# Performance work log

Hardware: AMD Instinct MI355X
Metric: run time of the kernel (lower is better)

## Reference

```python
import jax, jax.numpy as jnp
import numpy as np

EPS = 1e-5  # BatchNorm eps (torch default)

def _bn(x, gamma, beta):
    # training-mode BatchNorm over the edge/node (leading) axis, biased var
    mean = x.mean(axis=0, keepdims=True)
    var = x.var(axis=0, keepdims=True)
    return (x - mean) * jax.lax.rsqrt(var + EPS) * gamma + beta

def _silu(x):
    return x * jax.nn.sigmoid(x)

def setup_inputs() -> dict:
    N, E, H, NH = 50000, 800000, 128, 4
    HD = H // NH
    key = jax.random.key(0)
    ks = jax.random.split(key, 8)
    x = jax.random.normal(ks[0], (N, H), dtype=jnp.float32)
    weight = jax.random.uniform(ks[1], (N, 1), dtype=jnp.float32)  # positive fraction weights
    src = jax.random.randint(ks[2], (E,), 0, N)
    dst = jax.random.randint(ks[3], (E,), 0, N)
    # f: Linear(2H, 1) + BN(1)
    Wf = jax.random.normal(ks[4], (2 * H, 1), dtype=jnp.float32) * 0.05
    bf = jnp.zeros((1,), jnp.float32)
    f_gamma = jnp.ones((1,), jnp.float32)
    f_beta = jnp.zeros((1,), jnp.float32)
    # g: NH heads of Linear(2H, HD) + BN(HD), stacked on leading head axis
    Wg = jax.random.normal(ks[5], (NH, 2 * H, HD), dtype=jnp.float32) * 0.05
    bg = jnp.zeros((NH, HD), jnp.float32)
    g_gamma = jnp.ones((NH, HD), jnp.float32)
    g_beta = jnp.zeros((NH, HD), jnp.float32)
    # bn_nodes: BN(H)
    n_gamma = jnp.ones((H,), jnp.float32)
    n_beta = jnp.zeros((H,), jnp.float32)
    return dict(x=x, weight=weight, src=src, dst=dst, Wf=Wf, bf=bf,
                f_gamma=f_gamma, f_beta=f_beta, Wg=Wg, bg=bg,
                g_gamma=g_gamma, g_beta=g_beta, n_gamma=n_gamma, n_beta=n_beta)

def reference(x, weight, src, dst, Wf, bf, f_gamma, f_beta, Wg, bg, g_gamma, g_beta, n_gamma, n_beta):
    N = x.shape[0]
    E = src.shape[0]
    # per-edge concat of src/dst node features: [E, 2H]
    hihj = jnp.concatenate([x[src], x[dst]], axis=-1)
    # attention logit f(hihj) = SiLU(BN(Linear)) then exp: [E, 1]
    exp_e = jnp.exp(_silu(_bn(hihj @ Wf + bf, f_gamma, f_beta)))
    # weighted softmax-like normalization over incoming edges of each dst node
    we = weight[src] * exp_e                                   # [E, 1]
    sum_w_exp = jax.ops.segment_sum(we, dst, num_segments=N)   # [N, 1]
    a = we / sum_w_exp[dst]                                    # [E, 1]
    # multi-head message: a_ij * SiLU(BN(Linear_h(hihj))) per head, concat
    z = jnp.einsum('ed,hdk->ehk', hihj, Wg) + bg               # [E, NH, HD]
    z = _silu(_bn(z, g_gamma, g_beta))
    msg = (a[:, :, None] * z).reshape(E, -1)                   # [E, H]
    h = jax.ops.segment_sum(msg, dst, num_segments=N)          # [N, H]
    out = _bn(h, n_gamma, n_beta) + x                          # residual
    return out
```

## Files before the change

### kernel.cpp

```cpp
#include <hip/hip_runtime.h>
#include <hip/hip_bf16.h>
#include <math.h>

#define HDIM 128
#define PAD 64
#define CSTR 16
typedef unsigned short ushort_t;
typedef unsigned int uint_t;
typedef __attribute__((ext_vector_type(8))) short bf16x8;
typedef __attribute__((ext_vector_type(4))) float f32x4;
typedef __attribute__((ext_vector_type(2))) float v2f;

__device__ __forceinline__ float wave_allreduce(float v){
  #pragma unroll
  for (int o = 1; o < 64; o <<= 1) v += __shfl_xor(v, o);
  return v;
}

__device__ __forceinline__ ushort_t f2bf(float f){
  uint_t u = __float_as_uint(f);
  uint_t r = (u + 0x7fffu + ((u >> 16) & 1u)) >> 16;
  return (ushort_t)r;
}

__device__ __forceinline__ v2f bf2(uint_t u){
  v2f r;
  r.x = __uint_as_float(u << 16);
  r.y = __uint_as_float(u & 0xffff0000u);
  return r;
}

__global__ __launch_bounds__(128) void k_wpack(const float* __restrict__ Wg,
    const float* __restrict__ Wf, ushort_t* __restrict__ W3,
    int* __restrict__ cnt, int C){
  int b = blockIdx.x;
  int k = threadIdx.x;
  if (b < 272){
    float val;
    if (b < 128)       val = Wg[(size_t)(b >> 5) * 8192 + k * 32 + (b & 31)];
    else if (b < 256){ int c2 = b - 128;
                       val = Wg[(size_t)(c2 >> 5) * 8192 + (k + 128) * 32 + (c2 & 31)]; }
    else if (b == 256) val = Wf[k];
    else if (b == 257) val = Wf[128 + k];
    else               val = 0.f;
    int idx = (((b >> 4) * 4 + (k >> 5)) * 16 + (b & 15)) * 32 + (k & 31);
    W3[idx] = f2bf(val);
  } else {
    int i = (b - 272) * 128 + k;
    if (i < C) cnt[i] = 0;
  }
}

__global__ __launch_bounds__(256) void k_gemmfill(const float* __restrict__ x,
    const ushort_t* __restrict__ W3, const float* __restrict__ weight,
    ushort_t* __restrict__ Pb, ushort_t* __restrict__ Qb,
    float* __restrict__ v, float2* __restrict__ uw2,
    const int* __restrict__ src, const int* __restrict__ dst,
    int* __restrict__ cnt, int* __restrict__ es,
    int N, int E, int GB){
  __shared__ ushort_t xl[32 * 128];
  __shared__ ushort_t cl[32 * 264];
  if ((int)blockIdx.x < GB){
    int tid = threadIdx.x;
    int n_base = blockIdx.x * 32;
    #pragma unroll
    for (int i = 0; i < 4; ++i){
      int cidx = i * 256 + tid;
      int row = cidx >> 5, ch = cidx & 31;
      int rowc = n_base + row; rowc = rowc < N ? rowc : N - 1;
      float4 a = *(const float4*)(x + (size_t)rowc * HDIM + ch * 4);
      uint_t lo = (uint_t)f2bf(a.x) | ((uint_t)f2bf(a.y) << 16);
      uint_t hi = (uint_t)f2bf(a.z) | ((uint_t)f2bf(a.w) << 16);
      int bo = (row * 256 + ch * 8) ^ ((row & 7) << 4);
      *(uint2*)((char*)xl + bo) = make_uint2(lo, hi);
    }
    __syncthreads();
    int wid = __builtin_amdgcn_readfirstlane(tid >> 6);
    int lane = tid & 63;
    int quad = lane >> 4, col = lane & 15;
    int strip = wid >> 1;
    int half = wid & 1;
    int tbeg = half * 8;
    int ntile = half ? 9 : 8;
    f32x4 acc[9];
    #pragma unroll
    for (int t = 0; t < 9; ++t) acc[t] = (f32x4){0.f, 0.f, 0.f, 0.f};
    int arow = strip * 16 + col;
    #pragma unroll
    for (int kk = 0; kk < 4; ++kk){
      int abyte = (arow * 256 + kk * 64 + quad * 16) ^ ((col & 7) << 4);
      bf16x8 af = *(const bf16x8*)((char*)xl + abyte);
      const ushort_t* wb = W3 + (size_t)(tbeg * 4 + kk) * 512 + col * 32 + quad * 8;
      #pragma unroll
      for (int t = 0; t < 9; ++t){
        if (t < ntile){
          bf16x8 bfr = *(const bf16x8*)(wb + (size_t)t * 2048);
          acc[t] = __builtin_amdgcn_mfma_f32_16x16x32_bf16(af, bfr, acc[t], 0, 0, 0);
        }
      }
    }
    #pragma unroll
    for (int t = 0; t < 8; ++t){
      int ct = tbeg + t;
      #pragma unroll
      for (int r = 0; r < 4; ++r){
        int lr = strip * 16 + quad * 4 + r;
        cl[lr * 264 + ct * 16 + col] = f2bf(acc[t][r]);
      }
    }
    if (half){
      #pragma unroll
      for (int r = 0; r < 4; ++r){
        int n = n_base + strip * 16 + quad * 4 + r;
        if (n < N){
          float val = acc[8][r];
          if (col == 0)      uw2[n] = make_float2(val, weight[n]);
          else if (col == 1) v[n] = val;
        }
      }
    }
    __syncthreads();
    int row = tid >> 3, seg = tid & 7;
    int n = n_base + row;
    if (n < N){
      const ushort_t* s = cl + row * 264 + seg * 32;
      uint4 w0 = *(const uint4*)(s);
      uint4 w1 = *(const uint4*)(s + 8);
      uint4 w2 = *(const uint4*)(s + 16);
      uint4 w3v = *(const uint4*)(s + 24);
      if (seg < 4){
        ushort_t* dp = Pb + (size_t)n * HDIM + seg * 32;
        *(uint4*)(dp) = w0; *(uint4*)(dp + 8) = w1;
        *(uint4*)(dp + 16) = w2; *(uint4*)(dp + 24) = w3v;
      } else {
        ushort_t* dp = Qb + (size_t)n * HDIM + (seg - 4) * 32;
        *(uint4*)(dp) = w0; *(uint4*)(dp + 8) = w1;
        *(uint4*)(dp + 16) = w2; *(uint4*)(dp + 24) = w3v;
      }
    }
  } else {
    int bi = blockIdx.x - GB;
    int part = (int)blockIdx.x & 7;
    int nch = (gridDim.x - GB) >> 3;
    int chunk = bi >> 3;
    int Npp = (N + 7) >> 3;
    int lo = part * Npp;
    int hi = lo + Npp; if (hi > N) hi = N;
    int stride = nch * 256;
    int e = chunk * 256 + threadIdx.x;
#define FILL1(d, s) if ((d) >= lo && (d) < hi){ \
    int c = atomicAdd(&cnt[(size_t)(d) * CSTR], 1); \
    if (c < PAD) es[(size_t)(d) * PAD + c] = (s); }
    for (; e + 7 * stride < E; e += 8 * stride){
      int d0 = dst[e],            d1 = dst[e + stride];
      int d2 = dst[e + 2*stride], d3 = dst[e + 3*stride];
      int d4 = dst[e + 4*stride], d5 = dst[e + 5*stride];
      int d6 = dst[e + 6*stride], d7 = dst[e + 7*stride];
      int s0 = src[e],            s1 = src[e + stride];
      int s2 = src[e + 2*stride], s3 = src[e + 3*stride];
      int s4 = src[e + 4*stride], s5 = src[e + 5*stride];
      int s6 = src[e + 6*stride], s7 = src[e + 7*stride];
      FILL1(d0, s0) FILL1(d1, s1) FILL1(d2, s2) FILL1(d3, s3)
      FILL1(d4, s4) FILL1(d5, s5) FILL1(d6, s6) FILL1(d7, s7)
    }
    for (; e < E; e += stride){
      int d = dst[e];
      FILL1(d, src[e])
    }
#undef FILL1
  }
}

#define SH8(sjv,jj,S) \
  int S##0=__shfl(sjv,(jj)),   S##1=__shfl(sjv,(jj)+1), S##2=__shfl(sjv,(jj)+2), S##3=__shfl(sjv,(jj)+3), \
      S##4=__shfl(sjv,(jj)+4), S##5=__shfl(sjv,(jj)+5), S##6=__shfl(sjv,(jj)+6), S##7=__shfl(sjv,(jj)+7);
#define LD8(S,P) \
  uint_t P##0=Pu[(size_t)S##0*64+lane], P##1=Pu[(size_t)S##1*64+lane], \
         P##2=Pu[(size_t)S##2*64+lane], P##3=Pu[(size_t)S##3*64+lane], \
         P##4=Pu[(size_t)S##4*64+lane], P##5=Pu[(size_t)S##5*64+lane], \
         P##6=Pu[(size_t)S##6*64+lane], P##7=Pu[(size_t)S##7*64+lane];
#define SH4(sjv,jj,S) \
  int S##0=__shfl(sjv,(jj)),   S##1=__shfl(sjv,(jj)+1), S##2=__shfl(sjv,(jj)+2), S##3=__shfl(sjv,(jj)+3);
#define LD4(S,P) \
  uint_t P##0=Pu[(size_t)S##0*64+lane], P##1=Pu[(size_t)S##1*64+lane], \
         P##2=Pu[(size_t)S##2*64+lane], P##3=Pu[(size_t)S##3*64+lane];

__global__ __launch_bounds__(256) void k_gstats(const ushort_t* __restrict__ Pb,
    const ushort_t* __restrict__ Qb, const float* __restrict__ v,
    const float2* __restrict__ uw2, const int* __restrict__ es,
    const int* __restrict__ cnt, float* __restrict__ pstatG, int N){
  int lane = threadIdx.x & 63;
  int wid = __builtin_amdgcn_readfirstlane(threadIdx.x >> 6);
  int part = (int)blockIdx.x & 7;
  int Npp = (N + 7) >> 3;
  int lo = part * Npp;
  int hi = lo + Npp; if (hi > N) hi = N;
  int stp = (gridDim.x >> 3) << 2;
  const uint_t* Pu = (const uint_t*)Pb;
  const uint_t* Qu = (const uint_t*)Qb;
  v2f gs = {0.f,0.f}, gq = {0.f,0.f};
  float fs = 0.f, fq = 0.f;
  int n0 = lo + ((blockIdx.x >> 3) << 2) + wid;
  int n1 = n0 + stp;
  int dnA=0,sjA=0; uint_t qAu=0; float vA=0.f;
  int dnB=0,sjB=0; uint_t qBu=0; float vB=0.f;
  if (n0 < hi){ dnA=cnt[(size_t)n0*CSTR]; sjA=es[(size_t)n0*PAD+lane];
                qAu=Qu[(size_t)n0*64+lane]; vA=v[n0]; }
  if (n1 < hi){ dnB=cnt[(size_t)n1*CSTR]; sjB=es[(size_t)n1*PAD+lane];
                qBu=Qu[(size_t)n1*64+lane]; vB=v[n1]; }
#define GST(p,Sv,Qv) { v2f y=bf2(p); Sv+=y; Qv.x=fmaf(y.x,y.x,Qv.x); Qv.y=fmaf(y.y,y.y,Qv.y); }
#define GED8(P,Sv,Qv) GST(P##0,Sv,Qv) GST(P##1,Sv,Qv) GST(P##2,Sv,Qv) GST(P##3,Sv,Qv) \
                      GST(P##4,Sv,Qv) GST(P##5,Sv,Qv) GST(P##6,Sv,Qv) GST(P##7,Sv,Qv)
#define GED4(P,Sv,Qv) GST(P##0,Sv,Qv) GST(P##1,Sv,Qv) GST(P##2,Sv,Qv) GST(P##3,Sv,Qv)
  while (n0 < hi){
    int m0 = n0 + 2*stp, m1 = n1 + 2*stp;
    int dnC=0,sjC=0; uint_t qCu=0; float vC=0.f;
    int dnD=0,sjD=0; uint_t qDu=0; float vD=0.f;
    if (m0 < hi){ dnC=cnt[(size_t)m0*CSTR]; sjC=es[(size_t)m0*PAD+lane];
                  qCu=Qu[(size_t)m0*64+lane]; vC=v[m0]; }
    if (m1 < hi){ dnD=cnt[(size_t)m1*CSTR]; sjD=es[(size_t)m1*PAD+lane];
                  qDu=Qu[(size_t)m1*64+lane]; vD=v[m1]; }
    int dA = dnA < PAD ? dnA : PAD;
    int dB = (n1 < hi) ? (dnB < PAD ? dnB : PAD) : 0;
    if (lane < dA){ float2 uw = uw2[sjA]; float t = uw.x + vA; fs += t; fq = fmaf(t,t,fq); }
    if (lane < dB){ float2 uw = uw2[sjB]; float t = uw.x + vB; fs += t; fq = fmaf(t,t,fq); }
    v2f qa = bf2(qAu), qb = bf2(qBu);
    v2f SnA={0.f,0.f}, SSA={0.f,0.f}, SnB={0.f,0.f}, SSB={0.f,0.f};
    int j0 = 0, j1 = 0;
    for (; j0 + 7 < dA && j1 + 7 < dB; j0 += 8, j1 += 8){
      SH8(sjA,j0,xa) SH8(sjB,j1,xb)
      LD8(xa,pa) LD8(xb,pb)
      GED8(pa,SnA,SSA) GED8(pb,SnB,SSB)
    }
    for (; j0 + 7 < dA; j0 += 8){ SH8(sjA,j0,xa) LD8(xa,pa) GED8(pa,SnA,SSA) }
    for (; j0 + 3 < dA; j0 += 4){ SH4(sjA,j0,xa) LD4(xa,pa) GED4(pa,SnA,SSA) }
    for (; j0 < dA; ++j0){ int s0=__shfl(sjA,j0); uint_t p0=Pu[(size_t)s0*64+lane]; GST(p0,SnA,SSA) }
    for (; j1 + 7 < dB; j1 += 8){ SH8(sjB,j1,xb) LD8(xb,pb) GED8(pb,SnB,SSB) }
    for (; j1 + 3 < dB; j1 += 4){ SH4(sjB,j1,xb) LD4(xb,pb) GED4(pb,SnB,SSB) }
    for (; j1 < dB; ++j1){ int s0=__shfl(sjB,j1); uint_t p0=Pu[(size_t)s0*64+lane]; GST(p0,SnB,SSB) }
    float dAf = (float)dA, dBf = (float)dB;
    gs.x += SnA.x + SnB.x + dAf*qa.x + dBf*qb.x;
    gs.y += SnA.y + SnB.y + dAf*qa.y + dBf*qb.y;
    gq.x += SSA.x + SSB.x + qa.x*fmaf(dAf,qa.x,2.f*SnA.x) + qb.x*fmaf(dBf,qb.x,2.f*SnB.x);
    gq.y += SSA.y + SSB.y + qa.y*fmaf(dAf,qa.y,2.f*SnA.y) + qb.y*fmaf(dBf,qb.y,2.f*SnB.y);
    n0 = m0; n1 = m1;
    dnA=dnC; sjA=sjC; qAu=qCu; vA=vC;
    dnB=dnD; sjB=sjD; qBu=qDu; vB=vD;
  }
#undef GST
#undef GED8
#undef GED4
  fs = wave_allreduce(fs); fq = wave_allreduce(fq);
  __shared__ float red[4][258];
  red[wid][2*lane]       = gs.x; red[wid][2*lane+1]   = gs.y;
  red[wid][128+2*lane]   = gq.x; red[wid][129+2*lane] = gq.y;
  if (lane == 0){ red[wid][256] = fs; red[wid][257] = fq; }
  __syncthreads();
  for (int c = threadIdx.x; c < 258; c += 256)
    pstatG[(size_t)blockIdx.x * 258 + c] = red[0][c] + red[1][c] + red[2][c] + red[3][c];
}

__global__ __launch_bounds__(256) void k_redfin1(const float* __restrict__ pstatG,
    int NB, const float* __restrict__ g_gamma, const float* __restrict__ g_beta,
    const float* __restrict__ f_gamma, const float* __restrict__ f_beta,
    float* __restrict__ fin, long long E){
  int j = blockIdx.x;
  int c1 = (j < 128) ? j : 256;
  int c2 = (j < 128) ? 128 + j : 257;
  double s1 = 0, s2 = 0;
  for (int b = threadIdx.x; b < NB; b += 256){
    const float* pb = pstatG + (size_t)b * 258;
    s1 += (double)pb[c1]; s2 += (double)pb[c2];
  }
  __shared__ double m1[256], m2[256];
  m1[threadIdx.x] = s1; m2[threadIdx.x] = s2;
  __syncthreads();
  for (int o = 128; o; o >>= 1){
    if (threadIdx.x < o){ m1[threadIdx.x] += m1[threadIdx.x + o];
                          m2[threadIdx.x] += m2[threadIdx.x + o]; }
    __syncthreads();
  }
  if (threadIdx.x == 0){
    double m = m1[0] / (double)E;
    double var = m2[0] / (double)E - m * m;
    if (j < 128){
      float sc = (float)((double)g_gamma[j] / sqrt(var + 1e-5));
      fin[2 + j] = sc; fin[130 + j] = g_beta[j] - (float)m * sc;
    } else {
      float sc = (float)((double)f_gamma[0] / sqrt(var + 1e-5));
      fin[0] = sc; fin[1] = f_beta[0] - (float)m * sc;
    }
  }
}

__global__ __launch_bounds__(256) void k_msg(const ushort_t* __restrict__ Pb,
    const ushort_t* __restrict__ Qb, const float* __restrict__ v,
    const float2* __restrict__ uw2, const int* __restrict__ es,
    const int* __restrict__ cnt, const float* __restrict__ fin,
    float* __restrict__ h, float* __restrict__ pstatH, int N){
  int lane = threadIdx.x & 63;
  int wid = __builtin_amdgcn_readfirstlane(threadIdx.x >> 6);
  int part = (int)blockIdx.x & 7;
  int Npp = (N + 7) >> 3;
  int lo = part * Npp;
  int hi = lo + Npp; if (hi > N) hi = N;
  int stp = (gridDim.x >> 3) << 2;
  const uint_t* Pu = (const uint_t*)Pb;
  const uint_t* Qu = (const uint_t*)Qb;
  float fsc = fin[0], fsh = fin[1];
  v2f gsc = {fin[2 + 2*lane], fin[3 + 2*lane]};
  v2f gsh = {fin[130 + 2*lane], fin[131 + 2*lane]};
  v2f hs = {0.f,0.f}, hq = {0.f,0.f};
  int n0 = lo + ((blockIdx.x >> 3) << 2) + wid;
  int n1 = n0 + stp;
  int dnA=0,sjA=0; uint_t qAu=0; float vA=0.f;
  int dnB=0,sjB=0; uint_t qBu=0; float vB=0.f;
  if (n0 < hi){ dnA=cnt[(size_t)n0*CSTR]; sjA=es[(size_t)n0*PAD+lane];
                qAu=Qu[(size_t)n0*64+lane]; vA=v[n0]; }
  if (n1 < hi){ dnB=cnt[(size_t)n1*CSTR]; sjB=es[(size_t)n1*PAD+lane];
                qBu=Qu[(size_t)n1*64+lane]; vB=v[n1]; }
#define EDGE(p,a,qv,av) { v2f y = (bf2(p) + qv) * gsc + gsh; \
      float e0 = __expf(-y.x), e1 = __expf(-y.y); \
      float d0 = 1.f + e0, d1 = 1.f + e1; \
      float r = __builtin_amdgcn_rcpf(d0 * d1) * (a); \
      av.x = fmaf(y.x * d1, r, av.x); av.y = fmaf(y.y * d0, r, av.y); }
#define ASH8(wjv,jj,A) \
  float A##0=__shfl(wjv,(jj)),   A##1=__shfl(wjv,(jj)+1), A##2=__shfl(wjv,(jj)+2), A##3=__shfl(wjv,(jj)+3), \
        A##4=__shfl(wjv,(jj)+4), A##5=__shfl(wjv,(jj)+5), A##6=__shfl(wjv,(jj)+6), A##7=__shfl(wjv,(jj)+7);
#define ASH4(wjv,jj,A) \
  float A##0=__shfl(wjv,(jj)),   A##1=__shfl(wjv,(jj)+1), A##2=__shfl(wjv,(jj)+2), A##3=__shfl(wjv,(jj)+3);
#define MED8(P,A,qv,av) EDGE(P##0,A##0,qv,av) EDGE(P##1,A##1,qv,av) EDGE(P##2,A##2,qv,av) EDGE(P##3,A##3,qv,av) \
                        EDGE(P##4,A##4,qv,av) EDGE(P##5,A##5,qv,av) EDGE(P##6,A##6,qv,av) EDGE(P##7,A##7,qv,av)
#define MED4(P,A,qv,av) EDGE(P##0,A##0,qv,av) EDGE(P##1,A##1,qv,av) EDGE(P##2,A##2,qv,av) EDGE(P##3,A##3,qv,av)
  while (n0 < hi){
    int m0 = n0 + 2*stp, m1 = n1 + 2*stp;
    int dnC=0,sjC=0; uint_t qCu=0; float vC=0.f;
    int dnD=0,sjD=0; uint_t qDu=0; float vD=0.f;
    if (m0 < hi){ dnC=cnt[(size_t)m0*CSTR]; sjC=es[(size_t)m0*PAD+lane];
                  qCu=Qu[(size_t)m0*64+lane]; vC=v[m0]; }
    if (m1 < hi){ dnD=cnt[(size_t)m1*CSTR]; sjD=es[(size_t)m1*PAD+lane];
                  qDu=Qu[(size_t)m1*64+lane]; vD=v[m1]; }
    int dA = dnA < PAD ? dnA : PAD;
    int dB = (n1 < hi) ? (dnB < PAD ? dnB : PAD) : 0;
    float wjA = 0.f, wjB = 0.f;
    if (lane < dA){ float2 uw = uw2[sjA];
      float tt = fmaf(uw.x + vA, fsc, fsh);
      float sl = tt * __builtin_amdgcn_rcpf(1.f + __expf(-tt));
      wjA = uw.y * __expf(sl); }
    if (lane < dB){ float2 uw = uw2[sjB];
      float tt = fmaf(uw.x + vB, fsc, fsh);
      float sl = tt * __builtin_amdgcn_rcpf(1.f + __expf(-tt));
      wjB = uw.y * __expf(sl); }
    v2f qa = bf2(qAu), qb = bf2(qBu);
    v2f accA = {0.f,0.f}, accB = {0.f,0.f};
    int j0 = 0, j1 = 0;
    for (; j0 + 7 < dA && j1 + 7 < dB; j0 += 8, j1 += 8){
      SH8(sjA,j0,xa) SH8(sjB,j1,xb)
      ASH8(wjA,j0,aa) ASH8(wjB,j1,ab)
      LD8(xa,pa) LD8(xb,pb)
      MED8(pa,aa,qa,accA) MED8(pb,ab,qb,accB)
    }
    for (; j0 + 7 < dA; j0 += 8){ SH8(sjA,j0,xa) ASH8(wjA,j0,aa) LD8(xa,pa) MED8(pa,aa,qa,accA) }
    for (; j0 + 3 < dA; j0 += 4){ SH4(sjA,j0,xa) ASH4(wjA,j0,aa) LD4(xa,pa) MED4(pa,aa,qa,accA) }
    for (; j0 < dA; ++j0){ int s0=__shfl(sjA,j0); float a0=__shfl(wjA,j0);
                           uint_t p0=Pu[(size_t)s0*64+lane]; EDGE(p0,a0,qa,accA) }
    for (; j1 + 7 < dB; j1 += 8){ SH8(sjB,j1,xb) ASH8(wjB,j1,ab) LD8(xb,pb) MED8(pb,ab,qb,accB) }
    for (; j1 + 3 < dB; j1 += 4){ SH4(sjB,j1,xb) ASH4(wjB,j1,ab) LD4(xb,pb) MED4(pb,ab,qb,accB) }
    for (; j1 < dB; ++j1){ int s0=__shfl(sjB,j1); float a0=__shfl(wjB,j1);
                           uint_t p0=Pu[(size_t)s0*64+lane]; EDGE(p0,a0,qb,accB) }
    float swA = wjA, swB = wjB;
    #pragma unroll
    for (int o = 1; o < 64; o <<= 1){ swA += __shfl_xor(swA, o); swB += __shfl_xor(swB, o); }
    float rsA = (dA > 0) ? (1.f / swA) : 0.f;
    float rsB = (dB > 0) ? (1.f / swB) : 0.f;
    accA.x *= rsA; accA.y *= rsA;
    accB.x *= rsB; accB.y *= rsB;
    *(float2*)&h[(size_t)n0 * 128 + 2*lane] = make_float2(accA.x, accA.y);
    hs += accA; hq += accA * accA;
    if (n1 < hi){
      *(float2*)&h[(size_t)n1 * 128 + 2*lane] = make_float2(accB.x, accB.y);
      hs += accB; hq += accB * accB;
    }
    n0 = m0; n1 = m1;
    dnA=dnC; sjA=sjC; qAu=qCu; vA=vC;
    dnB=dnD; sjB=sjD; qBu=qDu; vB=vD;
  }
#undef EDGE
#undef ASH8
#undef ASH4
#undef MED8
#undef MED4
  __shared__ float red[4][256];
  red[wid][2*lane]       = hs.x; red[wid][2*lane+1]   = hs.y;
  red[wid][128+2*lane]   = hq.x; red[wid][129+2*lane] = hq.y;
  __syncthreads();
  int c = threadIdx.x;
  pstatH[(size_t)blockIdx.x * 256 + c] = red[0][c] + red[1][c] + red[2][c] + red[3][c];
}

__global__ __launch_bounds__(256) void k_redfin2(const float* __restrict__ pstatH,
    int NB, const float* __restrict__ n_gamma, const float* __restrict__ n_beta,
    float* __restrict__ fin, int N){
  int j = blockIdx.x;
  double s1 = 0, s2 = 0;
  for (int b = threadIdx.x; b < NB; b += 256){
    const float* pb = pstatH + (size_t)b * 256;
    s1 += (double)pb[j]; s2 += (double)pb[128 + j];
  }
  __shared__ double m1[256], m2[256];
  m1[threadIdx.x] = s1; m2[threadIdx.x] = s2;
  __syncthreads();
  for (int o = 128; o; o >>= 1){
    if (threadIdx.x < o){ m1[threadIdx.x] += m1[threadIdx.x + o];
                          m2[threadIdx.x] += m2[threadIdx.x + o]; }
    __syncthreads();
  }
  if (threadIdx.x == 0){
    double m = m1[0] / (double)N;
    double var = m2[0] / (double)N - m * m;
    float sc = (float)((double)n_gamma[j] / sqrt(var + 1e-5));
    fin[258 + j] = sc; fin[386 + j] = n_beta[j] - (float)m * sc;
  }
}

__global__ __launch_bounds__(256) void k_out(const float* __restrict__ h,
    const float* __restrict__ x, const float* __restrict__ fin,
    float* __restrict__ out, int total4){
  int i = blockIdx.x * 256 + threadIdx.x;
  if (i >= total4) return;
  const float4* h4 = (const float4*)h; const float4* x4 = (const float4*)x;
  float4 hv = h4[i], xv = x4[i];
  int c = (i * 4) & 127;
  float4 o;
  o.x = fmaf(hv.x, fin[258 + c],     fin[386 + c])     + xv.x;
  o.y = fmaf(hv.y, fin[258 + c + 1], fin[386 + c + 1]) + xv.y;
  o.z = fmaf(hv.z, fin[258 + c + 2], fin[386 + c + 2]) + xv.z;
  o.w = fmaf(hv.w, fin[258 + c + 3], fin[386 + c + 3]) + xv.w;
  ((float4*)out)[i] = o;
}

extern "C" void kernel_launch(void* const* d_in, const int* in_sizes, int n_in,
                              void* d_out, int out_size, void* d_ws, size_t ws_size,
                              hipStream_t stream){
  const float* x       = (const float*)d_in[0];
  const float* weight  = (const float*)d_in[1];
  const int*   src     = (const int*)d_in[2];
  const int*   dst     = (const int*)d_in[3];
  const float* Wf      = (const float*)d_in[4];
  const float* f_gamma = (const float*)d_in[6];
  const float* f_beta  = (const float*)d_in[7];
  const float* Wg      = (const float*)d_in[8];
  const float* g_gamma = (const float*)d_in[10];
  const float* g_beta  = (const float*)d_in[11];
  const float* n_gamma = (const float*)d_in[12];
  const float* n_beta  = (const float*)d_in[13];
  float* out = (float*)d_out;

  int N = in_sizes[0] / HDIM;
  int E = in_sizes[2];

  char* ws = (char*)d_ws;
  size_t off = 0;
  auto alloc = [&](size_t bytes)->char*{
    char* p = ws + off; off = (off + bytes + 255) & ~(size_t)255; return p;
  };
  ushort_t* Pb    = (ushort_t*)alloc((size_t)N * HDIM * 2);
  ushort_t* Qb    = (ushort_t*)alloc((size_t)N * HDIM * 2);
  float* h        = (float*)alloc((size_t)N * HDIM * 4);
  float* v        = (float*)alloc((size_t)N * 4);
  float2* uw2     = (float2*)alloc((size_t)N * 8);
  int* es         = (int*)alloc((size_t)N * PAD * 4);
  ushort_t* W3    = (ushort_t*)alloc((size_t)272 * 128 * 2);
  int* cnt        = (int*)alloc((size_t)N * CSTR * 4);
  const int NWB = 2048;
  const int NB  = NWB;
  float*  pstatG = (float*)alloc((size_t)NB * 258 * 4);
  float*  pstatH = (float*)alloc((size_t)NB * 256 * 4);
  float*  fin    = (float*)alloc(514 * 4);

  int GB = (N + 31) / 32;
  const int FB = 1024;
  int CT = N * CSTR;

  k_wpack   <<<272 + (CT + 127) / 128, 128, 0, stream>>>(Wg, Wf, W3, cnt, CT);
  k_gemmfill<<<GB + FB, 256, 0, stream>>>(x, W3, weight, Pb, Qb, v, uw2,
                                          src, dst, cnt, es, N, E, GB);
  k_gstats  <<<NWB, 256, 0, stream>>>(Pb, Qb, v, uw2, es, cnt, pstatG, N);
  k_redfin1 <<<129, 256, 0, stream>>>(pstatG, NB, g_gamma, g_beta, f_gamma, f_beta, fin, (long long)E);
  k_msg     <<<NWB, 256, 0, stream>>>(Pb, Qb, v, uw2, es, cnt, fin, h, pstatH, N);
  k_redfin2 <<<128, 256, 0, stream>>>(pstatH, NB, n_gamma, n_beta, fin, N);
  k_out     <<<(N * HDIM / 4 + 255) / 256, 256, 0, stream>>>(h, x, fin, out, N * HDIM / 4);
}
```

Before: 275.7 us.

## Restructure edge bucket fill to single pass with dense counters and vector loads

The edge-bucketing fill drops its 8-way dst-partitioned passes, where every fill block scanned all edges and filtered by node range. Each thread now handles 8 contiguous edges once, using int4 loads of src/dst. The counter array loses its 16-int per-node padding and becomes dense, which shrinks the zeroing work and the counter reads in later kernels. Fill blocks are scheduled before the GEMM blocks, and the gstats/msg grids drop from 2048 to 512 blocks. The trade-off is more atomic contention on dense counters and less L2 locality than the partitioned scheme had.

```diff
diff --git a/kernel.cpp b/kernel.cpp
--- a/kernel.cpp
+++ b/kernel.cpp
@@ -4,7 +4,6 @@
 
 #define HDIM 128
 #define PAD 64
-#define CSTR 16
 typedef unsigned short ushort_t;
 typedef unsigned int uint_t;
 typedef __attribute__((ext_vector_type(8))) short bf16x8;
@@ -57,12 +56,32 @@
     float* __restrict__ v, float2* __restrict__ uw2,
     const int* __restrict__ src, const int* __restrict__ dst,
     int* __restrict__ cnt, int* __restrict__ es,
-    int N, int E, int GB){
+    int N, int E, int FB){
   __shared__ ushort_t xl[32 * 128];
   __shared__ ushort_t cl[32 * 264];
-  if ((int)blockIdx.x < GB){
+  if ((int)blockIdx.x < FB){
+    int t = blockIdx.x * 256 + threadIdx.x;
+    int e0 = t * 8;
+#define FILL1(d, s) { \
+    int c = atomicAdd(&cnt[d], 1); \
+    if (c < PAD) es[(size_t)(d) * PAD + c] = (s); }
+    if (e0 + 8 <= E){
+      int4 da = *(const int4*)(dst + e0);
+      int4 db = *(const int4*)(dst + e0 + 4);
+      int4 sa = *(const int4*)(src + e0);
+      int4 sb = *(const int4*)(src + e0 + 4);
+      FILL1(da.x, sa.x) FILL1(da.y, sa.y) FILL1(da.z, sa.z) FILL1(da.w, sa.w)
+      FILL1(db.x, sb.x) FILL1(db.y, sb.y) FILL1(db.z, sb.z) FILL1(db.w, sb.w)
+    } else {
+      for (int e = e0; e < E; ++e){
+        int d = dst[e];
+        FILL1(d, src[e])
+      }
+    }
+#undef FILL1
+  } else {
     int tid = threadIdx.x;
-    int n_base = blockIdx.x * 32;
+    int n_base = ((int)blockIdx.x - FB) * 32;
     #pragma unroll
     for (int i = 0; i < 4; ++i){
       int cidx = i * 256 + tid;
@@ -138,36 +157,6 @@
         *(uint4*)(dp + 16) = w2; *(uint4*)(dp + 24) = w3v;
       }
     }
-  } else {
-    int bi = blockIdx.x - GB;
-    int part = (int)blockIdx.x & 7;
-    int nch = (gridDim.x - GB) >> 3;
-    int chunk = bi >> 3;
-    int Npp = (N + 7) >> 3;
-    int lo = part * Npp;
-    int hi = lo + Npp; if (hi > N) hi = N;
-    int stride = nch * 256;
-    int e = chunk * 256 + threadIdx.x;
-#define FILL1(d, s) if ((d) >= lo && (d) < hi){ \
-    int c = atomicAdd(&cnt[(size_t)(d) * CSTR], 1); \
-    if (c < PAD) es[(size_t)(d) * PAD + c] = (s); }
-    for (; e + 7 * stride < E; e += 8 * stride){
-      int d0 = dst[e],            d1 = dst[e + stride];
-      int d2 = dst[e + 2*stride], d3 = dst[e + 3*stride];
-      int d4 = dst[e + 4*stride], d5 = dst[e + 5*stride];
-      int d6 = dst[e + 6*stride], d7 = dst[e + 7*stride];
-      int s0 = src[e],            s1 = src[e + stride];
-      int s2 = src[e + 2*stride], s3 = src[e + 3*stride];
-      int s4 = src[e + 4*stride], s5 = src[e + 5*stride];
-      int s6 = src[e + 6*stride], s7 = src[e + 7*stride];
-      FILL1(d0, s0) FILL1(d1, s1) FILL1(d2, s2) FILL1(d3, s3)
-      FILL1(d4, s4) FILL1(d5, s5) FILL1(d6, s6) FILL1(d7, s7)
-    }
-    for (; e < E; e += stride){
-      int d = dst[e];
-      FILL1(d, src[e])
-    }
-#undef FILL1
   }
 }
 
@@ -204,9 +193,9 @@
   int n1 = n0 + stp;
   int dnA=0,sjA=0; uint_t qAu=0; float vA=0.f;
   int dnB=0,sjB=0; uint_t qBu=0; float vB=0.f;
-  if (n0 < hi){ dnA=cnt[(size_t)n0*CSTR]; sjA=es[(size_t)n0*PAD+lane];
+  if (n0 < hi){ dnA=cnt[n0]; sjA=es[(size_t)n0*PAD+lane];
                 qAu=Qu[(size_t)n0*64+lane]; vA=v[n0]; }
-  if (n1 < hi){ dnB=cnt[(size_t)n1*CSTR]; sjB=es[(size_t)n1*PAD+lane];
+  if (n1 < hi){ dnB=cnt[n1]; sjB=es[(size_t)n1*PAD+lane];
                 qBu=Qu[(size_t)n1*64+lane]; vB=v[n1]; }
 #define GST(p,Sv,Qv) { v2f y=bf2(p); Sv+=y; Qv.x=fmaf(y.x,y.x,Qv.x); Qv.y=fmaf(y.y,y.y,Qv.y); }
 #define GED8(P,Sv,Qv) GST(P##0,Sv,Qv) GST(P##1,Sv,Qv) GST(P##2,Sv,Qv) GST(P##3,Sv,Qv) \
@@ -216,9 +205,9 @@
     int m0 = n0 + 2*stp, m1 = n1 + 2*stp;
     int dnC=0,sjC=0; uint_t qCu=0; float vC=0.f;
     int dnD=0,sjD=0; uint_t qDu=0; float vD=0.f;
-    if (m0 < hi){ dnC=cnt[(size_t)m0*CSTR]; sjC=es[(size_t)m0*PAD+lane];
+    if (m0 < hi){ dnC=cnt[m0]; sjC=es[(size_t)m0*PAD+lane];
                   qCu=Qu[(size_t)m0*64+lane]; vC=v[m0]; }
-    if (m1 < hi){ dnD=cnt[(size_t)m1*CSTR]; sjD=es[(size_t)m1*PAD+lane];
+    if (m1 < hi){ dnD=cnt[m1]; sjD=es[(size_t)m1*PAD+lane];
                   qDu=Qu[(size_t)m1*64+lane]; vD=v[m1]; }
     int dA = dnA < PAD ? dnA : PAD;
     int dB = (n1 < hi) ? (dnB < PAD ? dnB : PAD) : 0;
@@ -315,9 +304,9 @@
   int n1 = n0 + stp;
   int dnA=0,sjA=0; uint_t qAu=0; float vA=0.f;
   int dnB=0,sjB=0; uint_t qBu=0; float vB=0.f;
-  if (n0 < hi){ dnA=cnt[(size_t)n0*CSTR]; sjA=es[(size_t)n0*PAD+lane];
+  if (n0 < hi){ dnA=cnt[n0]; sjA=es[(size_t)n0*PAD+lane];
                 qAu=Qu[(size_t)n0*64+lane]; vA=v[n0]; }
-  if (n1 < hi){ dnB=cnt[(size_t)n1*CSTR]; sjB=es[(size_t)n1*PAD+lane];
+  if (n1 < hi){ dnB=cnt[n1]; sjB=es[(size_t)n1*PAD+lane];
                 qBu=Qu[(size_t)n1*64+lane]; vB=v[n1]; }
 #define EDGE(p,a,qv,av) { v2f y = (bf2(p) + qv) * gsc + gsh; \
       float e0 = __expf(-y.x), e1 = __expf(-y.y); \
@@ -336,9 +325,9 @@
     int m0 = n0 + 2*stp, m1 = n1 + 2*stp;
     int dnC=0,sjC=0; uint_t qCu=0; float vC=0.f;
     int dnD=0,sjD=0; uint_t qDu=0; float vD=0.f;
-    if (m0 < hi){ dnC=cnt[(size_t)m0*CSTR]; sjC=es[(size_t)m0*PAD+lane];
+    if (m0 < hi){ dnC=cnt[m0]; sjC=es[(size_t)m0*PAD+lane];
                   qCu=Qu[(size_t)m0*64+lane]; vC=v[m0]; }
-    if (m1 < hi){ dnD=cnt[(size_t)m1*CSTR]; sjD=es[(size_t)m1*PAD+lane];
+    if (m1 < hi){ dnD=cnt[m1]; sjD=es[(size_t)m1*PAD+lane];
                   qDu=Qu[(size_t)m1*64+lane]; vD=v[m1]; }
     int dA = dnA < PAD ? dnA : PAD;
     int dB = (n1 < hi) ? (dnB < PAD ? dnB : PAD) : 0;
@@ -471,20 +460,19 @@
   float2* uw2     = (float2*)alloc((size_t)N * 8);
   int* es         = (int*)alloc((size_t)N * PAD * 4);
   ushort_t* W3    = (ushort_t*)alloc((size_t)272 * 128 * 2);
-  int* cnt        = (int*)alloc((size_t)N * CSTR * 4);
-  const int NWB = 2048;
+  int* cnt        = (int*)alloc((size_t)N * 4);
+  const int NWB = 512;
   const int NB  = NWB;
   float*  pstatG = (float*)alloc((size_t)NB * 258 * 4);
   float*  pstatH = (float*)alloc((size_t)NB * 256 * 4);
   float*  fin    = (float*)alloc(514 * 4);
 
   int GB = (N + 31) / 32;
-  const int FB = 1024;
-  int CT = N * CSTR;
-
-  k_wpack   <<<272 + (CT + 127) / 128, 128, 0, stream>>>(Wg, Wf, W3, cnt, CT);
-  k_gemmfill<<<GB + FB, 256, 0, stream>>>(x, W3, weight, Pb, Qb, v, uw2,
-                                          src, dst, cnt, es, N, E, GB);
+  int FB = (E + 2047) / 2048;
+
+  k_wpack   <<<272 + (N + 127) / 128, 128, 0, stream>>>(Wg, Wf, W3, cnt, N);
+  k_gemmfill<<<FB + GB, 256, 0, stream>>>(x, W3, weight, Pb, Qb, v, uw2,
+                                          src, dst, cnt, es, N, E, FB);
   k_gstats  <<<NWB, 256, 0, stream>>>(Pb, Qb, v, uw2, es, cnt, pstatG, N);
   k_redfin1 <<<129, 256, 0, stream>>>(pstatG, NB, g_gamma, g_beta, f_gamma, f_beta, fin, (long long)E);
   k_msg     <<<NWB, 256, 0, stream>>>(Pb, Qb, v, uw2, es, cnt, fin, h, pstatH, N);
```

Result: slower. 303.1 us (+9.9%).
